# Performance work log

Hardware: AMD Instinct MI355X
Metric: run time of the kernel (lower is better)

Reference implementation:

```python
import jax, jax.numpy as jnp
import numpy as np

B, S, H, E, I_E, V = 4, 4096, 1024, 8, 512, 100000


def setup_inputs() -> dict:
    key = jax.random.key(0)
    k0, k1, k2, k3, k4, k5, k6 = jax.random.split(key, 7)
    hidden_states = jax.random.normal(k0, (B, S, H), dtype=jnp.float32)
    token_ids = jax.random.randint(k1, (B, S), 0, V, dtype=jnp.int64)
    mu = jax.random.normal(k2, (B, S, H), dtype=jnp.float32)
    # torch Linear(in,out,bias=False) weight is [out,in]; we store transposed [in,out]
    w_gate = jax.random.normal(k3, (E, H, I_E), dtype=jnp.float32) * 0.02
    w_up = jax.random.normal(k4, (E, H, I_E), dtype=jnp.float32) * 0.02
    w_down = jax.random.normal(k5, (E, I_E, H), dtype=jnp.float32) * 0.02
    # module zero-inits mu_router; use small random so the mu-override path is exercised
    mu_router_w = jax.random.normal(k6, (E, H), dtype=jnp.float32) * 0.02
    return {
        "hidden_states": hidden_states,
        "token_ids": token_ids,
        "mu": mu,
        "w_gate": w_gate,
        "w_up": w_up,
        "w_down": w_down,
        "mu_router_w": mu_router_w,
    }


def reference(hidden_states, token_ids, mu, w_gate, w_up, w_down, mu_router_w):
    num_experts = w_gate.shape[0]
    # deterministic token->expert mapping: token_id % num_experts (after clamp)
    tid = jnp.clip(token_ids, 0, V - 1)
    base_expert_ids = (tid % num_experts).astype(jnp.int32)  # [B,S]
    # mu-guided override: one_hot*10 + mu_logits, argmax
    mu_logits = jnp.einsum("bsh,eh->bse", mu, mu_router_w)
    base_one_hot = jax.nn.one_hot(base_expert_ids, num_experts, dtype=mu_logits.dtype)
    expert_ids = jnp.argmax(base_one_hot * 10.0 + mu_logits, axis=-1)  # [B,S]

    x = hidden_states.reshape(-1, H)          # [T,H], T=B*S
    eid = expert_ids.reshape(-1)              # [T]
    out = jnp.zeros_like(x)
    for e in range(num_experts):
        mask = (eid == e)[:, None]            # [T,1]
        g = x @ w_gate[e]                     # [T,I_E]
        u = x @ w_up[e]                       # [T,I_E]
        y = (jax.nn.silu(g) * u) @ w_down[e]  # [T,H] SwiGLU
        out = out + jnp.where(mask, y, 0.0)
    return out.reshape(hidden_states.shape)
```

## Files before the change

### kernel.cpp

```cpp
#include <hip/hip_runtime.h>
#include <stdint.h>

#define T_TOK   16384
#define H_DIM   1024
#define IE_DIM  512
#define E_NUM   8
#define V_MAX   100000

typedef __attribute__((ext_vector_type(8))) short bf16x8;
typedef __attribute__((ext_vector_type(4))) float f32x4;
typedef unsigned long long ull;

__device__ __forceinline__ unsigned short f2bf(float f) {
  union { float f; unsigned u; } v; v.f = f;
  unsigned r = v.u + 0x7fffu + ((v.u >> 16) & 1u);
  return (unsigned short)(r >> 16);
}

__device__ __forceinline__ void gload16(const void* g, void* l) {
  __builtin_amdgcn_global_load_lds(
      (const __attribute__((address_space(1))) unsigned int*)g,
      (__attribute__((address_space(3))) unsigned int*)(unsigned int)(uintptr_t)l,
      16, 0, 0);
}

__global__ __launch_bounds__(256) void k_pre(
    const float* __restrict__ mu, const int* __restrict__ tok,
    const float* __restrict__ mrw, int* __restrict__ eid,
    int* __restrict__ blockCnt,
    const float* __restrict__ wg, const float* __restrict__ wu,
    const float* __restrict__ wd, unsigned short* __restrict__ WgT,
    unsigned short* __restrict__ WuT, unsigned short* __restrict__ WdT) {
  __shared__ unsigned short lds[64][72];
  int tid = threadIdx.x;

  if (blockIdx.x < 1024) {
    int* cnt = (int*)&lds[0][0];
    if (tid < 8) cnt[tid] = 0;
    int wv = blockIdx.x * 4 + (tid >> 6);
    int t0 = wv * 4;
    int lane = tid & 63;
    const float4* mrw4 = (const float4*)mrw;

    float acc[4][E_NUM];
#pragma unroll
    for (int i = 0; i < 4; i++)
#pragma unroll
      for (int e = 0; e < E_NUM; e++) acc[i][e] = 0.f;

#pragma unroll
    for (int j = 0; j < 4; j++) {
      int idx = lane + 64 * j;
      float4 wr[E_NUM];
#pragma unroll
      for (int e = 0; e < E_NUM; e++) wr[e] = mrw4[e * 256 + idx];
#pragma unroll
      for (int i = 0; i < 4; i++) {
        float4 m = ((const float4*)(mu + (size_t)(t0 + i) * H_DIM))[idx];
#pragma unroll
        for (int e = 0; e < E_NUM; e++)
          acc[i][e] += m.x * wr[e].x + m.y * wr[e].y + m.z * wr[e].z + m.w * wr[e].w;
      }
    }
#pragma unroll
    for (int i = 0; i < 4; i++)
#pragma unroll
      for (int e = 0; e < E_NUM; e++)
#pragma unroll
        for (int off = 32; off >= 1; off >>= 1)
          acc[i][e] += __shfl_xor(acc[i][e], off, 64);

    __syncthreads();
#pragma unroll
    for (int i = 0; i < 4; i++) {
      int tv = tok[t0 + i];
      if (tv < 0) tv = 0;
      if (tv > V_MAX - 1) tv = V_MAX - 1;
      int base = tv & 7;
      int best = 0; float bs = -1e30f;
#pragma unroll
      for (int e = 0; e < E_NUM; e++) {
        float s = acc[i][e] + (e == base ? 10.f : 0.f);
        if (s > bs) { bs = s; best = e; }
      }
      if (lane == i) {
        eid[t0 + i] = best;
        atomicAdd(&cnt[best], 1);
      }
    }
    __syncthreads();
    if (tid < 8) blockCnt[blockIdx.x * 8 + tid] = cnt[tid];
  } else {
    int sel = (blockIdx.x - 1024) >> 10;
    int blk = blockIdx.x & 1023;
    const float* src; unsigned short* dst; int R, C;
    if (sel == 0)      { src = wg; dst = WgT; R = H_DIM; C = IE_DIM; }
    else if (sel == 1) { src = wu; dst = WuT; R = H_DIM; C = IE_DIM; }
    else               { src = wd; dst = WdT; R = IE_DIM; C = H_DIM; }
    int tpe = (R >> 6) * (C >> 6);
    int e = blk / tpe;
    int rem = blk % tpe;
    int tr = rem / (C >> 6);
    int tc = rem % (C >> 6);
    const float* s = src + (size_t)e * R * C;
    unsigned short* d = dst + (size_t)e * R * C;
    int r0 = tid >> 4;
    int c0 = (tid & 15) * 4;
#pragma unroll
    for (int i = 0; i < 4; i++) {
      int r = r0 + i * 16;
      float4 v = *(const float4*)(s + (size_t)(tr * 64 + r) * C + tc * 64 + c0);
      lds[r][c0 + 0] = f2bf(v.x); lds[r][c0 + 1] = f2bf(v.y);
      lds[r][c0 + 2] = f2bf(v.z); lds[r][c0 + 3] = f2bf(v.w);
    }
    __syncthreads();
    int oc = tid >> 2;
    int ob = (tid & 3) * 16;
    unsigned short tmp[16];
#pragma unroll
    for (int i = 0; i < 16; i++) tmp[i] = lds[ob + i][oc];
    uint4* dp = (uint4*)(d + (size_t)(tc * 64 + oc) * R + tr * 64 + ob);
    dp[0] = ((uint4*)tmp)[0];
    dp[1] = ((uint4*)tmp)[1];
  }
}

__global__ __launch_bounds__(1024) void k_scan2(
    const int* __restrict__ blockCnt, int* __restrict__ blockBase,
    int* __restrict__ offsets, int* __restrict__ tileOff) {
  int b = threadIdx.x;
  __shared__ ull s0[1024], s1[1024];
  __shared__ int offL[8];
  const int4* p = (const int4*)(blockCnt + b * 8);
  int4 x0 = p[0], x1 = p[1];
  int c[8] = {x0.x, x0.y, x0.z, x0.w, x1.x, x1.y, x1.z, x1.w};
  ull v0 = (ull)c[0] | ((ull)c[1] << 16) | ((ull)c[2] << 32) | ((ull)c[3] << 48);
  ull v1 = (ull)c[4] | ((ull)c[5] << 16) | ((ull)c[6] << 32) | ((ull)c[7] << 48);
  s0[b] = v0; s1[b] = v1;
  __syncthreads();
  for (int st = 1; st < 1024; st <<= 1) {
    ull a0 = 0, a1 = 0;
    if (b >= st) { a0 = s0[b - st]; a1 = s1[b - st]; }
    __syncthreads();
    v0 += a0; v1 += a1;
    s0[b] = v0; s1[b] = v1;
    __syncthreads();
  }
  if (b == 1023) {
    int tot[8];
#pragma unroll
    for (int e = 0; e < 4; e++) tot[e] = (int)((v0 >> (16 * e)) & 0xFFFF);
#pragma unroll
    for (int e = 0; e < 4; e++) tot[4 + e] = (int)((v1 >> (16 * e)) & 0xFFFF);
    int s = 0, ts = 0;
    for (int e = 0; e < E_NUM; e++) {
      offsets[e] = s; offL[e] = s; tileOff[e] = ts;
      s += tot[e];
      ts += (tot[e] + 127) >> 7;
    }
    offsets[E_NUM] = s; tileOff[E_NUM] = ts;
  }
  __syncthreads();
  int be[8];
#pragma unroll
  for (int e = 0; e < 4; e++)
    be[e] = offL[e] + (int)((v0 >> (16 * e)) & 0xFFFF) - c[e];
#pragma unroll
  for (int e = 0; e < 4; e++)
    be[4 + e] = offL[4 + e] + (int)((v1 >> (16 * e)) & 0xFFFF) - c[4 + e];
  int4* q = (int4*)(blockBase + b * 8);
  q[0] = make_int4(be[0], be[1], be[2], be[3]);
  q[1] = make_int4(be[4], be[5], be[6], be[7]);
}

__global__ __launch_bounds__(256) void k_gather(
    const float* __restrict__ hs, const int* __restrict__ eid,
    const int* __restrict__ blockBase, int* __restrict__ tokofrow,
    unsigned short* __restrict__ Xs) {
  int b = blockIdx.x;
  int tid = threadIdx.x;
  __shared__ int eL[16];
  __shared__ int posL[16];
  if (tid < 16) eL[tid] = eid[b * 16 + tid];
  __syncthreads();
  if (tid < 16) {
    int e = eL[tid];
    int r = 0;
    for (int j = 0; j < tid; j++) r += (eL[j] == e);
    int pos = blockBase[b * 8 + e] + r;
    posL[tid] = pos;
    tokofrow[pos] = b * 16 + tid;
  }
  __syncthreads();
  int w = tid >> 6, lane = tid & 63;
#pragma unroll
  for (int i = 0; i < 4; i++) {
    int li = w * 4 + i;
    int t = b * 16 + li;
    int pos = posL[li];
    const float4* src = (const float4*)(hs + (size_t)t * H_DIM);
    unsigned short* drow = Xs + (size_t)pos * H_DIM;
#pragma unroll
    for (int j = 0; j < 4; j++) {
      float4 v = src[lane + 64 * j];
      ushort4 bb;
      bb.x = f2bf(v.x); bb.y = f2bf(v.y); bb.z = f2bf(v.z); bb.w = f2bf(v.w);
      *(ushort4*)(drow + (lane + 64 * j) * 4) = bb;
    }
  }
}

__global__ __launch_bounds__(512) void k_gemm1(
    const unsigned short* __restrict__ Xs,
    const unsigned short* __restrict__ WgT,
    const unsigned short* __restrict__ WuT,
    unsigned short* __restrict__ Hb,
    const int* __restrict__ offsets, const int* __restrict__ tileOff) {
  int nt = blockIdx.x & 3;
  int mlin = blockIdx.x >> 2;
  if (mlin >= tileOff[E_NUM]) return;
  int e = 0;
#pragma unroll
  for (int i = 1; i < E_NUM; i++)
    if (mlin >= tileOff[i]) e = i;
  int mtile = mlin - tileOff[e];
  int segStart = offsets[e], segEnd = offsets[e + 1];
  int M = segEnd - segStart;

  __shared__ unsigned short Alds[2][128 * 32];
  __shared__ unsigned short Bglds[2][128 * 32];
  __shared__ unsigned short Bulds[2][128 * 32];

  int tid = threadIdx.x;
  int lane = tid & 63;
  int w = tid >> 6;
  int wm = w >> 2;
  int wn = w & 3;

  f32x4 accg[4][2], accu[4][2];
#pragma unroll
  for (int i = 0; i < 4; i++)
#pragma unroll
    for (int j = 0; j < 2; j++) {
      accg[i][j] = (f32x4)(0.f);
      accu[i][j] = (f32x4)(0.f);
    }

  int sr = tid >> 2;
  int sc = tid & 3;
  int scc = sc ^ ((sr >> 1) & 3);
  int grow = mtile * 128 + sr;
  if (grow > M - 1) grow = M - 1;
  const unsigned short* Arow = Xs + (size_t)(segStart + grow) * H_DIM + scc * 8;
  const unsigned short* Bgrow =
      WgT + (size_t)e * IE_DIM * H_DIM + (size_t)(nt * 128 + sr) * H_DIM + scc * 8;
  const unsigned short* Burow =
      WuT + (size_t)e * IE_DIM * H_DIM + (size_t)(nt * 128 + sr) * H_DIM + scc * 8;

#define STAGE1(buf, k0)                                            \
  {                                                                \
    gload16(Arow + (k0), (char*)Alds[buf] + tid * 16);             \
    gload16(Bgrow + (k0), (char*)Bglds[buf] + tid * 16);           \
    gload16(Burow + (k0), (char*)Bulds[buf] + tid * 16);           \
  }

  int kc = lane >> 4;
  int arow[4], brow[2];
#pragma unroll
  for (int mf = 0; mf < 4; mf++) arow[mf] = wm * 64 + mf * 16 + (lane & 15);
#pragma unroll
  for (int nf = 0; nf < 2; nf++) brow[nf] = wn * 32 + nf * 16 + (lane & 15);

  STAGE1(0, 0);
  __syncthreads();

  const int NT = H_DIM / 32;
  int cur = 0;
  for (int t = 0; t < NT; t++) {
    if (t + 1 < NT) STAGE1(cur ^ 1, (t + 1) * 32);
    bf16x8 a[4], bg[2], bu[2];
#pragma unroll
    for (int mf = 0; mf < 4; mf++) {
      int row = arow[mf];
      int byte = row * 64 + ((kc ^ ((row >> 1) & 3)) << 4);
      a[mf] = *(const bf16x8*)((const char*)Alds[cur] + byte);
    }
#pragma unroll
    for (int nf = 0; nf < 2; nf++) {
      int row = brow[nf];
      int byte = row * 64 + ((kc ^ ((row >> 1) & 3)) << 4);
      bg[nf] = *(const bf16x8*)((const char*)Bglds[cur] + byte);
      bu[nf] = *(const bf16x8*)((const char*)Bulds[cur] + byte);
    }
#pragma unroll
    for (int mf = 0; mf < 4; mf++)
#pragma unroll
      for (int nf = 0; nf < 2; nf++) {
        accg[mf][nf] = __builtin_amdgcn_mfma_f32_16x16x32_bf16(
            a[mf], bg[nf], accg[mf][nf], 0, 0, 0);
        accu[mf][nf] = __builtin_amdgcn_mfma_f32_16x16x32_bf16(
            a[mf], bu[nf], accu[mf][nf], 0, 0, 0);
      }
    __syncthreads();
    cur ^= 1;
  }
#undef STAGE1

  int rowBase = segStart + mtile * 128 + wm * 64;
#pragma unroll
  for (int mf = 0; mf < 4; mf++)
#pragma unroll
    for (int nf = 0; nf < 2; nf++) {
      int col = nt * 128 + wn * 32 + nf * 16 + (lane & 15);
#pragma unroll
      for (int j = 0; j < 4; j++) {
        int r = rowBase + mf * 16 + (lane >> 4) * 4 + j;
        if (r < segEnd) {
          float g = accg[mf][nf][j];
          float u = accu[mf][nf][j];
          float h = (g / (1.f + __expf(-g))) * u;
          Hb[(size_t)r * IE_DIM + col] = f2bf(h);
        }
      }
    }
}

__global__ __launch_bounds__(512) void k_gemm2(
    const unsigned short* __restrict__ Hb,
    const unsigned short* __restrict__ WdT,
    float* __restrict__ out,
    const int* __restrict__ offsets, const int* __restrict__ tileOff,
    const int* __restrict__ tokofrow) {
  int nt = blockIdx.x & 7;
  int mlin = blockIdx.x >> 3;
  if (mlin >= tileOff[E_NUM]) return;
  int e = 0;
#pragma unroll
  for (int i = 1; i < E_NUM; i++)
    if (mlin >= tileOff[i]) e = i;
  int mtile = mlin - tileOff[e];
  int segStart = offsets[e], segEnd = offsets[e + 1];
  int M = segEnd - segStart;

  __shared__ unsigned short Alds[2][128 * 32];
  __shared__ unsigned short Blds[2][128 * 32];

  int tid = threadIdx.x;
  int lane = tid & 63;
  int w = tid >> 6;
  int wm = w >> 2;
  int wn = w & 3;

  f32x4 acc[4][2];
#pragma unroll
  for (int i = 0; i < 4; i++)
#pragma unroll
    for (int j = 0; j < 2; j++) acc[i][j] = (f32x4)(0.f);

  int sr = tid >> 2;
  int sc = tid & 3;
  int scc = sc ^ ((sr >> 1) & 3);
  int grow = mtile * 128 + sr;
  if (grow > M - 1) grow = M - 1;
  const unsigned short* Arow = Hb + (size_t)(segStart + grow) * IE_DIM + scc * 8;
  const unsigned short* Brow =
      WdT + (size_t)e * H_DIM * IE_DIM + (size_t)(nt * 128 + sr) * IE_DIM + scc * 8;

#define STAGE2(buf, k0)                                            \
  {                                                                \
    gload16(Arow + (k0), (char*)Alds[buf] + tid * 16);             \
    gload16(Brow + (k0), (char*)Blds[buf] + tid * 16);             \
  }

  int kc = lane >> 4;
  int arow[4], brow[2];
#pragma unroll
  for (int mf = 0; mf < 4; mf++) arow[mf] = wm * 64 + mf * 16 + (lane & 15);
#pragma unroll
  for (int nf = 0; nf < 2; nf++) brow[nf] = wn * 32 + nf * 16 + (lane & 15);

  STAGE2(0, 0);
  __syncthreads();

  const int NT = IE_DIM / 32;
  int cur = 0;
  for (int t = 0; t < NT; t++) {
    if (t + 1 < NT) STAGE2(cur ^ 1, (t + 1) * 32);
    bf16x8 a[4], b[2];
#pragma unroll
    for (int mf = 0; mf < 4; mf++) {
      int row = arow[mf];
      int byte = row * 64 + ((kc ^ ((row >> 1) & 3)) << 4);
      a[mf] = *(const bf16x8*)((const char*)Alds[cur] + byte);
    }
#pragma unroll
    for (int nf = 0; nf < 2; nf++) {
      int row = brow[nf];
      int byte = row * 64 + ((kc ^ ((row >> 1) & 3)) << 4);
      b[nf] = *(const bf16x8*)((const char*)Blds[cur] + byte);
    }
#pragma unroll
    for (int mf = 0; mf < 4; mf++)
#pragma unroll
      for (int nf = 0; nf < 2; nf++)
        acc[mf][nf] = __builtin_amdgcn_mfma_f32_16x16x32_bf16(
            a[mf], b[nf], acc[mf][nf], 0, 0, 0);
    __syncthreads();
    cur ^= 1;
  }
#undef STAGE2

  int rowBase = segStart + mtile * 128 + wm * 64;
#pragma unroll
  for (int mf = 0; mf < 4; mf++)
#pragma unroll
    for (int nf = 0; nf < 2; nf++) {
      int col = nt * 128 + wn * 32 + nf * 16 + (lane & 15);
#pragma unroll
      for (int j = 0; j < 4; j++) {
        int r = rowBase + mf * 16 + (lane >> 4) * 4 + j;
        if (r < segEnd) {
          int t = tokofrow[r];
          out[(size_t)t * H_DIM + col] = acc[mf][nf][j];
        }
      }
    }
}

#define WS_XS    ((size_t)0)
#define WS_WGT   ((size_t)33554432)
#define WS_WUT   ((size_t)41943040)
#define WS_WDT   ((size_t)50331648)
#define WS_HB    ((size_t)58720256)
#define WS_EID   ((size_t)75497472)
#define WS_TOK   ((size_t)75563008)
#define WS_OFF   ((size_t)75628544)
#define WS_BC    ((size_t)75629568)
#define WS_BB    ((size_t)75662336)

extern "C" void kernel_launch(void* const* d_in, const int* in_sizes, int n_in,
                              void* d_out, int out_size, void* d_ws, size_t ws_size,
                              hipStream_t stream) {
  const float* hs  = (const float*)d_in[0];
  const int*   tok = (const int*)d_in[1];
  const float* mu  = (const float*)d_in[2];
  const float* wg  = (const float*)d_in[3];
  const float* wu  = (const float*)d_in[4];
  const float* wd  = (const float*)d_in[5];
  const float* mrw = (const float*)d_in[6];
  float* out = (float*)d_out;
  char* ws = (char*)d_ws;

  unsigned short* Xs  = (unsigned short*)(ws + WS_XS);
  unsigned short* WgT = (unsigned short*)(ws + WS_WGT);
  unsigned short* WuT = (unsigned short*)(ws + WS_WUT);
  unsigned short* WdT = (unsigned short*)(ws + WS_WDT);
  unsigned short* Hb  = (unsigned short*)(ws + WS_HB);
  int* eid      = (int*)(ws + WS_EID);
  int* tokofrow = (int*)(ws + WS_TOK);
  int* offsets  = (int*)(ws + WS_OFF);
  int* tileOff  = offsets + 16;
  int* blockCnt = (int*)(ws + WS_BC);
  int* blockBase= (int*)(ws + WS_BB);

  k_pre<<<4096, 256, 0, stream>>>(mu, tok, mrw, eid, blockCnt,
                                  wg, wu, wd, WgT, WuT, WdT);
  k_scan2<<<1, 1024, 0, stream>>>(blockCnt, blockBase, offsets, tileOff);
  k_gather<<<1024, 256, 0, stream>>>(hs, eid, blockBase, tokofrow, Xs);
  k_gemm1<<<135 * 4, 512, 0, stream>>>(Xs, WgT, WuT, Hb, offsets, tileOff);
  k_gemm2<<<135 * 8, 512, 0, stream>>>(Hb, WdT, out, offsets, tileOff, tokofrow);
}
```

Before: 162.9 us.

## Triple-buffer LDS in both expert GEMMs with one barrier per k-step

Both grouped GEMM kernels move from double to triple LDS buffering. Two tiles are prefetched up front, and each iteration waits on vmcnt for the oldest tile and takes one barrier before issuing the load two steps ahead, replacing the trailing __syncthreads. This is meant to hide global-to-LDS latency better and halve barrier count. In exchange LDS use grows by half, which may reduce occupancy. The wrapped prefetch (tn modulo NT) issues redundant loads in the last two iterations into buffers that are no longer read.

```diff
diff --git a/kernel.cpp b/kernel.cpp
--- a/kernel.cpp
+++ b/kernel.cpp
@@ -227,9 +227,9 @@
   int segStart = offsets[e], segEnd = offsets[e + 1];
   int M = segEnd - segStart;
 
-  __shared__ unsigned short Alds[2][128 * 32];
-  __shared__ unsigned short Bglds[2][128 * 32];
-  __shared__ unsigned short Bulds[2][128 * 32];
+  __shared__ unsigned short Alds[3][128 * 32];
+  __shared__ unsigned short Bglds[3][128 * 32];
+  __shared__ unsigned short Bulds[3][128 * 32];
 
   int tid = threadIdx.x;
   int lane = tid & 63;
@@ -265,19 +265,25 @@
   }
 
   int kc = lane >> 4;
-  int arow[4], brow[2];
+  int arow[4], browv[2];
 #pragma unroll
   for (int mf = 0; mf < 4; mf++) arow[mf] = wm * 64 + mf * 16 + (lane & 15);
 #pragma unroll
-  for (int nf = 0; nf < 2; nf++) brow[nf] = wn * 32 + nf * 16 + (lane & 15);
-
+  for (int nf = 0; nf < 2; nf++) browv[nf] = wn * 32 + nf * 16 + (lane & 15);
+
+  const int NT = H_DIM / 32;
   STAGE1(0, 0);
-  __syncthreads();
-
-  const int NT = H_DIM / 32;
+  STAGE1(1, 32);
+
   int cur = 0;
   for (int t = 0; t < NT; t++) {
-    if (t + 1 < NT) STAGE1(cur ^ 1, (t + 1) * 32);
+    asm volatile("s_waitcnt vmcnt(3)" ::: "memory");
+    __builtin_amdgcn_s_barrier();
+    __builtin_amdgcn_sched_barrier(0);
+    int tn = t + 2; if (tn >= NT) tn -= NT;
+    int nbuf = cur + 2; if (nbuf >= 3) nbuf -= 3;
+    STAGE1(nbuf, tn * 32);
+
     bf16x8 a[4], bg[2], bu[2];
 #pragma unroll
     for (int mf = 0; mf < 4; mf++) {
@@ -287,7 +293,7 @@
     }
 #pragma unroll
     for (int nf = 0; nf < 2; nf++) {
-      int row = brow[nf];
+      int row = browv[nf];
       int byte = row * 64 + ((kc ^ ((row >> 1) & 3)) << 4);
       bg[nf] = *(const bf16x8*)((const char*)Bglds[cur] + byte);
       bu[nf] = *(const bf16x8*)((const char*)Bulds[cur] + byte);
@@ -301,10 +307,10 @@
         accu[mf][nf] = __builtin_amdgcn_mfma_f32_16x16x32_bf16(
             a[mf], bu[nf], accu[mf][nf], 0, 0, 0);
       }
-    __syncthreads();
-    cur ^= 1;
+    cur = (cur + 1 == 3) ? 0 : cur + 1;
   }
 #undef STAGE1
+  asm volatile("s_waitcnt vmcnt(0)" ::: "memory");
 
   int rowBase = segStart + mtile * 128 + wm * 64;
 #pragma unroll
@@ -342,8 +348,8 @@
   int segStart = offsets[e], segEnd = offsets[e + 1];
   int M = segEnd - segStart;
 
-  __shared__ unsigned short Alds[2][128 * 32];
-  __shared__ unsigned short Blds[2][128 * 32];
+  __shared__ unsigned short Alds[3][128 * 32];
+  __shared__ unsigned short Blds[3][128 * 32];
 
   int tid = threadIdx.x;
   int lane = tid & 63;
@@ -373,19 +379,25 @@
   }
 
   int kc = lane >> 4;
-  int arow[4], brow[2];
+  int arow[4], browv[2];
 #pragma unroll
   for (int mf = 0; mf < 4; mf++) arow[mf] = wm * 64 + mf * 16 + (lane & 15);
 #pragma unroll
-  for (int nf = 0; nf < 2; nf++) brow[nf] = wn * 32 + nf * 16 + (lane & 15);
-
+  for (int nf = 0; nf < 2; nf++) browv[nf] = wn * 32 + nf * 16 + (lane & 15);
+
+  const int NT = IE_DIM / 32;
   STAGE2(0, 0);
-  __syncthreads();
-
-  const int NT = IE_DIM / 32;
+  STAGE2(1, 32);
+
   int cur = 0;
   for (int t = 0; t < NT; t++) {
-    if (t + 1 < NT) STAGE2(cur ^ 1, (t + 1) * 32);
+    asm volatile("s_waitcnt vmcnt(2)" ::: "memory");
+    __builtin_amdgcn_s_barrier();
+    __builtin_amdgcn_sched_barrier(0);
+    int tn = t + 2; if (tn >= NT) tn -= NT;
+    int nbuf = cur + 2; if (nbuf >= 3) nbuf -= 3;
+    STAGE2(nbuf, tn * 32);
+
     bf16x8 a[4], b[2];
 #pragma unroll
     for (int mf = 0; mf < 4; mf++) {
@@ -395,7 +407,7 @@
     }
 #pragma unroll
     for (int nf = 0; nf < 2; nf++) {
-      int row = brow[nf];
+      int row = browv[nf];
       int byte = row * 64 + ((kc ^ ((row >> 1) & 3)) << 4);
       b[nf] = *(const bf16x8*)((const char*)Blds[cur] + byte);
     }
@@ -405,10 +417,10 @@
       for (int nf = 0; nf < 2; nf++)
         acc[mf][nf] = __builtin_amdgcn_mfma_f32_16x16x32_bf16(
             a[mf], b[nf], acc[mf][nf], 0, 0, 0);
-    __syncthreads();
-    cur ^= 1;
+    cur = (cur + 1 == 3) ? 0 : cur + 1;
   }
 #undef STAGE2
+  asm volatile("s_waitcnt vmcnt(0)" ::: "memory");
 
   int rowBase = segStart + mtile * 128 + wm * 64;
 #pragma unroll
```

New measurement: 162.0 us. No clear change (-0.5%).
